# Optimization experiments

Hardware: AMD Instinct MI355X
Metric: run time of the kernel (lower is better)

Reference implementation:

```python
import jax, jax.numpy as jnp
import numpy as np

WEIGHT = 1.0
EPS = 1e-10


def _high_mask(h, w):
    # Boolean mask: True = high-frequency region (outside center rectangle after fftshift)
    mask = np.ones((h, w), dtype=np.float32)
    ch, cw = h // 2, w // 2
    mask[ch - h // 8: ch + h // 8, cw - w // 8: cw + w // 8] = 0.0
    return jnp.asarray(mask)


def _high_freq_psd(img):
    # img: (B, 3, H, W) in [-1, 1] -> per-image mean log10 PSD over high-freq region, shape (B,)
    gray = 0.299 * img[:, 0] + 0.587 * img[:, 1] + 0.114 * img[:, 2]  # (B, H, W)
    gray = (gray + 1.0) / 2.0
    fft = jnp.fft.fft2(gray)                       # batched complex FFT over last two dims
    fft = jnp.fft.fftshift(fft, axes=(-2, -1))
    psd_log = jnp.log10(jnp.abs(fft) ** 2 + EPS)   # (B, H, W)
    h, w = gray.shape[-2:]
    mask = _high_mask(h, w)
    return jnp.sum(psd_log * mask, axis=(-2, -1)) / jnp.sum(mask)


def setup_inputs() -> dict:
    key = jax.random.key(0)
    k1, k2 = jax.random.split(key)
    B, C, H, W = 32, 3, 512, 512
    generated = jax.random.normal(k1, (B, C, H, W), dtype=jnp.float32)
    target = jax.random.normal(k2, (B, C, H, W), dtype=jnp.float32)
    return {"generated": generated, "target": target}


def reference(generated, target):
    psd_gen = _high_freq_psd(generated)      # (B,)
    psd_target = _high_freq_psd(target)      # (B,)
    loss = jnp.mean(jnp.abs(psd_gen - psd_target))  # F.l1_loss
    return WEIGHT * loss
```

## Files before the change

kernel.cpp:

```cpp
#include <hip/hip_runtime.h>
#include <hip/hip_bf16.h>
#include <math.h>


__device__ double g_partials[64 * 33 * 4];
__device__ __align__(16) float2 g_wsfall[256 * 512];

__device__ __forceinline__ float2 cadd(float2 a, float2 b){ return make_float2(a.x+b.x, a.y+b.y); }
__device__ __forceinline__ float2 csub(float2 a, float2 b){ return make_float2(a.x-b.x, a.y-b.y); }
__device__ __forceinline__ float2 cmul(float2 a, float2 b){
  return make_float2(fmaf(a.x, b.x, -(a.y*b.y)), fmaf(a.x, b.y, a.y*b.x));
}
__device__ __forceinline__ float2 mul_mi(float2 a){ return make_float2(a.y, -a.x); }

__device__ __forceinline__ void fft8(float2 v[8]){
  const float S = 0.70710678118654752440f;
  float2 c0=cadd(v[0],v[4]), c1=cadd(v[1],v[5]), c2=cadd(v[2],v[6]), c3=cadd(v[3],v[7]);
  float2 d0=csub(v[0],v[4]);
  float2 t1=csub(v[1],v[5]);
  float2 d1=make_float2(S*(t1.x+t1.y), S*(t1.y-t1.x));
  float2 d2=mul_mi(csub(v[2],v[6]));
  float2 t3=csub(v[3],v[7]);
  float2 d3=make_float2(S*(t3.y-t3.x), -S*(t3.x+t3.y));
  float2 e0=cadd(c0,c2), e1=cadd(c1,c3), f0=csub(c0,c2), f1=mul_mi(csub(c1,c3));
  float2 g0=cadd(d0,d2), g1=cadd(d1,d3), h0=csub(d0,d2), h1=mul_mi(csub(d1,d3));
  v[0]=cadd(e0,e1); v[4]=csub(e0,e1);
  v[2]=cadd(f0,f1); v[6]=csub(f0,f1);
  v[1]=cadd(g0,g1); v[5]=csub(g0,g1);
  v[3]=cadd(h0,h1); v[7]=csub(h0,h1);
}

__device__ __forceinline__ void twiddle8(float2 v[8], float ang){
  float sn, cs;
  __sincosf(ang, &sn, &cs);
  float2 w = make_float2(cs, sn);
  float2 wp = w;
  v[1] = cmul(v[1], wp);
  #pragma unroll
  for (int m = 2; m < 8; ++m){ wp = cmul(wp, w); v[m] = cmul(v[m], wp); }
}

__device__ __forceinline__ int padi(int i){ return i + (i >> 3); }

__device__ __forceinline__ void lds_fence(){
  asm volatile("s_waitcnt lgkmcnt(0)" ::: "memory");
  __builtin_amdgcn_sched_barrier(0);
}

__device__ __forceinline__ void fft512(float2 v[8], float* re, float* im, int t){
  const float TW = -6.28318530717958647692f;
  fft8(v);
  twiddle8(v, TW * (float)t * (1.0f/512.0f));
  lds_fence();
  #pragma unroll
  for (int m = 0; m < 8; ++m){ int a = padi(m*64 + t); re[a] = v[m].x; im[a] = v[m].y; }
  lds_fence();
  const int q = t >> 3, n = t & 7;
  #pragma unroll
  for (int j = 0; j < 8; ++j){ int a = padi(q*64 + n + 8*j); v[j].x = re[a]; v[j].y = im[a]; }
  fft8(v);
  twiddle8(v, TW * (float)n * (1.0f/64.0f));
  lds_fence();
  #pragma unroll
  for (int m = 0; m < 8; ++m){ int a = padi(q*64 + m*8 + n); re[a] = v[m].x; im[a] = v[m].y; }
  lds_fence();
  #pragma unroll
  for (int j = 0; j < 8; ++j){ int a = padi(q*64 + n*8 + j); v[j].x = re[a]; v[j].y = im[a]; }
  fft8(v);
}

#define GRAY1(r,g,b) ((fmaf(0.299f,(r), fmaf(0.587f,(g), 0.114f*(b))) + 1.0f)*0.5f)

__global__ __launch_bounds__(256, 4)
void k_rowfft(const float* __restrict__ gen, const float* __restrict__ tgt,
              float2* ws, int img0){
  float2* w = ws ? ws : g_wsfall;
  const int wg   = blockIdx.x;
  const int imgl = wg >> 6;
  const int rg   = wg & 63;
  const int img  = img0 + imgl;
  const int wave = threadIdx.x >> 6, t = threadIdx.x & 63;
  const int pr   = rg*4 + wave;
  const float* src = (img < 32) ? gen : tgt;
  const float4* f4 = (const float4*)(src + (size_t)(img & 31) * 786432) + (size_t)pr * 256 + t;

  __shared__ float re_all[4][576], im_all[4][576];
  float* re = re_all[wave];
  float* im = im_all[wave];

  float4 aR0 = f4[0],          aR1 = f4[64];
  float4 bR0 = f4[128],        bR1 = f4[192];
  float4 aG0 = f4[65536],      aG1 = f4[65536+64];
  float4 bG0 = f4[65536+128],  bG1 = f4[65536+192];
  float4 aB0 = f4[131072],     aB1 = f4[131072+64];
  float4 bB0 = f4[131072+128], bB1 = f4[131072+192];

  const int x0 = 4*t, x1 = 256 + 4*t;
  re[padi(x0+0)] = GRAY1(aR0.x, aG0.x, aB0.x);
  re[padi(x0+1)] = GRAY1(aR0.y, aG0.y, aB0.y);
  re[padi(x0+2)] = GRAY1(aR0.z, aG0.z, aB0.z);
  re[padi(x0+3)] = GRAY1(aR0.w, aG0.w, aB0.w);
  re[padi(x1+0)] = GRAY1(aR1.x, aG1.x, aB1.x);
  re[padi(x1+1)] = GRAY1(aR1.y, aG1.y, aB1.y);
  re[padi(x1+2)] = GRAY1(aR1.z, aG1.z, aB1.z);
  re[padi(x1+3)] = GRAY1(aR1.w, aG1.w, aB1.w);
  im[padi(x0+0)] = GRAY1(bR0.x, bG0.x, bB0.x);
  im[padi(x0+1)] = GRAY1(bR0.y, bG0.y, bB0.y);
  im[padi(x0+2)] = GRAY1(bR0.z, bG0.z, bB0.z);
  im[padi(x0+3)] = GRAY1(bR0.w, bG0.w, bB0.w);
  im[padi(x1+0)] = GRAY1(bR1.x, bG1.x, bB1.x);
  im[padi(x1+1)] = GRAY1(bR1.y, bG1.y, bB1.y);
  im[padi(x1+2)] = GRAY1(bR1.z, bG1.z, bB1.z);
  im[padi(x1+3)] = GRAY1(bR1.w, bG1.w, bB1.w);
  lds_fence();

  float2 v[8];
  #pragma unroll
  for (int j = 0; j < 8; ++j){
    const int a = padi(t + 64*j);
    v[j].x = re[a];
    v[j].y = im[a];
  }
  fft512(v, re, im, t);

  float2* dst = w + ((size_t)imgl * 256 + pr) * 512;
  const int off = 8*(t & 7) + (t >> 3);
  #pragma unroll
  for (int j = 0; j < 8; ++j) dst[64*j + off] = v[j];
}

__global__ __launch_bounds__(256)
void k_colfft(const float2* __restrict__ ws, int img0){
  const float2* w = ws ? ws : (const float2*)g_wsfall;
  const int wg   = blockIdx.x;
  const int imgl = wg / 33;
  const int blk  = wg - imgl * 33;
  const int img  = img0 + imgl;
  const int kx0  = blk * 8;
  const int tid  = threadIdx.x;
  const int wave = tid >> 6, t = tid & 63;
  const int ncols = (blk == 32) ? 1 : 8;

  __shared__ float2 own[8][260], mir[8][260];
  __shared__ float re_all[4][576], im_all[4][576];
  float* re = re_all[wave];
  float* im = im_all[wave];

  const float2* zb = w + (size_t)imgl * 131072;
  #pragma unroll
  for (int it = 0; it < 8; ++it){
    const int idx = it*256 + tid;
    const int p = idx >> 3, e = idx & 7;
    own[e][p] = zb[p*512 + kx0 + e];
    mir[e][p] = zb[p*512 + ((512 - (kx0 + e)) & 511)];
  }
  __syncthreads();

  double acc = 0.0;
  for (int ci = 0; ci < 2; ++ci){
    const int e = wave*2 + ci;
    if (e < ncols){
      const int kx = kx0 + e;
      const bool sub_own = (kx <= 63);
      const bool sub_mir = (kx >= 1) & (kx <= 64);
      const float base = (kx == 0 || kx == 256) ? 1.0f : 2.0f;

      float2 v[8];
      const int u = t >> 1;
      const bool odd = (t & 1);
      #pragma unroll
      for (int j = 0; j < 8; ++j){
        const int p = u + 32*j;
        float2 A = own[e][p];
        float2 B = mir[e][p]; B.y = -B.y;
        float2 Fe = make_float2((A.x + B.x)*0.5f, (A.y + B.y)*0.5f);
        float2 Fo = mul_mi(make_float2((A.x - B.x)*0.5f, (A.y - B.y)*0.5f));
        v[j] = odd ? Fo : Fe;
      }
      fft512(v, re, im, t);

      #pragma unroll
      for (int j = 0; j < 8; ++j){
        const bool inS  = (j == 0) | (j == 7);
        const bool inSp = (j == 0) | ((j == 1) & (t == 0)) | ((j == 7) & (t != 0));
        float wgt = base;
        if (sub_own & inS)  wgt -= 1.0f;
        if (sub_mir & inSp) wgt -= 1.0f;
        float m2 = fmaf(v[j].x, v[j].x, fmaf(v[j].y, v[j].y, 1e-10f));
        acc += (double)wgt * (double)log10f(m2);
      }
    }
  }
  #pragma unroll
  for (int off = 32; off; off >>= 1) acc += __shfl_down(acc, off);
  if (t == 0) g_partials[((size_t)img * 33 + blk) * 4 + wave] = acc;
}

__global__ __launch_bounds__(256)
void k_finish(float* __restrict__ out){
  const int tid = threadIdx.x;
  const int img = tid >> 2, part = tid & 3;
  const double* p = g_partials + (size_t)img * 132 + part;
  double s = 0.0;
  for (int k = 0; k < 33; ++k) s += p[4*k];
  __shared__ double sm[256];
  sm[tid] = s;
  __syncthreads();
  if ((tid & 3) == 0){
    double tot = sm[tid] + sm[tid+1] + sm[tid+2] + sm[tid+3];
    sm[tid] = tot * (1.0 / 245760.0);
  }
  __syncthreads();
  if (tid < 64){
    double dv = (tid < 32) ? fabs(sm[tid*4] - sm[(tid+32)*4]) : 0.0;
    #pragma unroll
    for (int off = 32; off; off >>= 1) dv += __shfl_down(dv, off);
    if (tid == 0) out[0] = (float)(dv * (1.0 / 32.0));
  }
}

extern "C" void kernel_launch(void* const* d_in, const int* in_sizes, int n_in,
                              void* d_out, int out_size, void* d_ws, size_t ws_size,
                              hipStream_t stream){
  (void)in_sizes; (void)n_in; (void)out_size;
  const float* gen = (const float*)d_in[0];
  const float* tgt = (const float*)d_in[1];
  float* out = (float*)d_out;

  const size_t per_img = (size_t)256 * 512 * sizeof(float2);
  int chunk = (int)(ws_size / per_img);
  float2* wsp = (float2*)d_ws;
  if (chunk < 1){ chunk = 1; wsp = nullptr; }
  if (chunk > 64) chunk = 64;

  for (int i0 = 0; i0 < 64; i0 += chunk){
    const int n = (64 - i0 < chunk) ? (64 - i0) : chunk;
    k_rowfft<<<dim3(n * 64), dim3(256), 0, stream>>>(gen, tgt, wsp, i0);
    k_colfft<<<dim3(n * 33), dim3(256), 0, stream>>>(wsp, i0);
  }
  k_finish<<<dim3(1), dim3(256), 0, stream>>>(out);
}
```

Before: 76.23 us.

## Process two row pairs per wave in row FFT with shared twiddles

The row-FFT kernel now has each wave transform two packed complex row pairs at once through a dual fft512, sharing one sincos per stage across both. Grayscale results are written to LDS with vectorized float4 stores. The grid is halved and launch bounds drop to 2 blocks per SM. The aim is more instruction-level parallelism and more outstanding global loads per wave, with less twiddle computation and fewer blocks to launch. The cost is higher register and LDS use per block, which lowers occupancy. The column kernel only inlines its FFT using the new twiddle helper.

```diff
diff --git a/kernel.cpp b/kernel.cpp
--- a/kernel.cpp
+++ b/kernel.cpp
@@ -30,10 +30,7 @@
   v[3]=cadd(h0,h1); v[7]=csub(h0,h1);
 }
 
-__device__ __forceinline__ void twiddle8(float2 v[8], float ang){
-  float sn, cs;
-  __sincosf(ang, &sn, &cs);
-  float2 w = make_float2(cs, sn);
+__device__ __forceinline__ void twiddle8w(float2 v[8], float2 w){
   float2 wp = w;
   v[1] = cmul(v[1], wp);
   #pragma unroll
@@ -47,86 +44,114 @@
   __builtin_amdgcn_sched_barrier(0);
 }
 
-__device__ __forceinline__ void fft512(float2 v[8], float* re, float* im, int t){
+__device__ __forceinline__ void fft512x2(float2 va[8], float2 vb[8],
+                                         float* rea, float* ima,
+                                         float* reb, float* imb, int t){
   const float TW = -6.28318530717958647692f;
-  fft8(v);
-  twiddle8(v, TW * (float)t * (1.0f/512.0f));
-  lds_fence();
-  #pragma unroll
-  for (int m = 0; m < 8; ++m){ int a = padi(m*64 + t); re[a] = v[m].x; im[a] = v[m].y; }
+  float sn, cs;
+  fft8(va); fft8(vb);
+  __sincosf(TW * (float)t * (1.0f/512.0f), &sn, &cs);
+  { float2 w = make_float2(cs, sn); twiddle8w(va, w); twiddle8w(vb, w); }
+  lds_fence();
+  #pragma unroll
+  for (int m = 0; m < 8; ++m){
+    int a = padi(m*64 + t);
+    rea[a] = va[m].x; ima[a] = va[m].y;
+    reb[a] = vb[m].x; imb[a] = vb[m].y;
+  }
   lds_fence();
   const int q = t >> 3, n = t & 7;
   #pragma unroll
-  for (int j = 0; j < 8; ++j){ int a = padi(q*64 + n + 8*j); v[j].x = re[a]; v[j].y = im[a]; }
-  fft8(v);
-  twiddle8(v, TW * (float)n * (1.0f/64.0f));
-  lds_fence();
-  #pragma unroll
-  for (int m = 0; m < 8; ++m){ int a = padi(q*64 + m*8 + n); re[a] = v[m].x; im[a] = v[m].y; }
-  lds_fence();
-  #pragma unroll
-  for (int j = 0; j < 8; ++j){ int a = padi(q*64 + n*8 + j); v[j].x = re[a]; v[j].y = im[a]; }
-  fft8(v);
+  for (int j = 0; j < 8; ++j){
+    int a = padi(q*64 + n + 8*j);
+    va[j].x = rea[a]; va[j].y = ima[a];
+    vb[j].x = reb[a]; vb[j].y = imb[a];
+  }
+  fft8(va); fft8(vb);
+  __sincosf(TW * (float)n * (1.0f/64.0f), &sn, &cs);
+  { float2 w = make_float2(cs, sn); twiddle8w(va, w); twiddle8w(vb, w); }
+  lds_fence();
+  #pragma unroll
+  for (int m = 0; m < 8; ++m){
+    int a = padi(q*64 + m*8 + n);
+    rea[a] = va[m].x; ima[a] = va[m].y;
+    reb[a] = vb[m].x; imb[a] = vb[m].y;
+  }
+  lds_fence();
+  #pragma unroll
+  for (int j = 0; j < 8; ++j){
+    int a = padi(q*64 + n*8 + j);
+    va[j].x = rea[a]; va[j].y = ima[a];
+    vb[j].x = reb[a]; vb[j].y = imb[a];
+  }
+  fft8(va); fft8(vb);
 }
 
 #define GRAY1(r,g,b) ((fmaf(0.299f,(r), fmaf(0.587f,(g), 0.114f*(b))) + 1.0f)*0.5f)
-
-__global__ __launch_bounds__(256, 4)
+__device__ __forceinline__ float4 gray4(float4 r, float4 g, float4 b){
+  return make_float4(GRAY1(r.x,g.x,b.x), GRAY1(r.y,g.y,b.y),
+                     GRAY1(r.z,g.z,b.z), GRAY1(r.w,g.w,b.w));
+}
+
+__global__ __launch_bounds__(256, 2)
 void k_rowfft(const float* __restrict__ gen, const float* __restrict__ tgt,
               float2* ws, int img0){
   float2* w = ws ? ws : g_wsfall;
   const int wg   = blockIdx.x;
-  const int imgl = wg >> 6;
-  const int rg   = wg & 63;
+  const int imgl = wg >> 5;
+  const int rg   = wg & 31;
   const int img  = img0 + imgl;
   const int wave = threadIdx.x >> 6, t = threadIdx.x & 63;
-  const int pr   = rg*4 + wave;
+  const int prA  = rg*8 + wave*2;
+  const int prB  = prA + 1;
   const float* src = (img < 32) ? gen : tgt;
-  const float4* f4 = (const float4*)(src + (size_t)(img & 31) * 786432) + (size_t)pr * 256 + t;
-
-  __shared__ float re_all[4][576], im_all[4][576];
-  float* re = re_all[wave];
-  float* im = im_all[wave];
-
-  float4 aR0 = f4[0],          aR1 = f4[64];
-  float4 bR0 = f4[128],        bR1 = f4[192];
-  float4 aG0 = f4[65536],      aG1 = f4[65536+64];
-  float4 bG0 = f4[65536+128],  bG1 = f4[65536+192];
-  float4 aB0 = f4[131072],     aB1 = f4[131072+64];
-  float4 bB0 = f4[131072+128], bB1 = f4[131072+192];
-
-  const int x0 = 4*t, x1 = 256 + 4*t;
-  re[padi(x0+0)] = GRAY1(aR0.x, aG0.x, aB0.x);
-  re[padi(x0+1)] = GRAY1(aR0.y, aG0.y, aB0.y);
-  re[padi(x0+2)] = GRAY1(aR0.z, aG0.z, aB0.z);
-  re[padi(x0+3)] = GRAY1(aR0.w, aG0.w, aB0.w);
-  re[padi(x1+0)] = GRAY1(aR1.x, aG1.x, aB1.x);
-  re[padi(x1+1)] = GRAY1(aR1.y, aG1.y, aB1.y);
-  re[padi(x1+2)] = GRAY1(aR1.z, aG1.z, aB1.z);
-  re[padi(x1+3)] = GRAY1(aR1.w, aG1.w, aB1.w);
-  im[padi(x0+0)] = GRAY1(bR0.x, bG0.x, bB0.x);
-  im[padi(x0+1)] = GRAY1(bR0.y, bG0.y, bB0.y);
-  im[padi(x0+2)] = GRAY1(bR0.z, bG0.z, bB0.z);
-  im[padi(x0+3)] = GRAY1(bR0.w, bG0.w, bB0.w);
-  im[padi(x1+0)] = GRAY1(bR1.x, bG1.x, bB1.x);
-  im[padi(x1+1)] = GRAY1(bR1.y, bG1.y, bB1.y);
-  im[padi(x1+2)] = GRAY1(bR1.z, bG1.z, bB1.z);
-  im[padi(x1+3)] = GRAY1(bR1.w, bG1.w, bB1.w);
-  lds_fence();
-
-  float2 v[8];
-  #pragma unroll
-  for (int j = 0; j < 8; ++j){
-    const int a = padi(t + 64*j);
-    v[j].x = re[a];
-    v[j].y = im[a];
-  }
-  fft512(v, re, im, t);
-
-  float2* dst = w + ((size_t)imgl * 256 + pr) * 512;
+  const float4* f4 = (const float4*)(src + (size_t)(img & 31) * 786432);
+  const float4* fA = f4 + (size_t)prA * 256 + t;
+  const float4* fB = f4 + (size_t)prB * 256 + t;
+
+  __shared__ float ex[4][4][576];
+  float* reA = ex[wave][0]; float* imA = ex[wave][1];
+  float* reB = ex[wave][2]; float* imB = ex[wave][3];
+
+  float4 ArR0 = fA[0],             ArR1 = fA[64];
+  float4 AsR0 = fA[128],           AsR1 = fA[192];
+  float4 ArG0 = fA[65536],         ArG1 = fA[65536+64];
+  float4 AsG0 = fA[65536+128],     AsG1 = fA[65536+192];
+  float4 ArB0 = fA[131072],        ArB1 = fA[131072+64];
+  float4 AsB0 = fA[131072+128],    AsB1 = fA[131072+192];
+  float4 BrR0 = fB[0],             BrR1 = fB[64];
+  float4 BsR0 = fB[128],           BsR1 = fB[192];
+  float4 BrG0 = fB[65536],         BrG1 = fB[65536+64];
+  float4 BsG0 = fB[65536+128],     BsG1 = fB[65536+192];
+  float4 BrB0 = fB[131072],        BrB1 = fB[131072+64];
+  float4 BsB0 = fB[131072+128],    BsB1 = fB[131072+192];
+
+  ((float4*)reA)[t]      = gray4(ArR0, ArG0, ArB0);
+  ((float4*)reA)[64 + t] = gray4(ArR1, ArG1, ArB1);
+  ((float4*)imA)[t]      = gray4(AsR0, AsG0, AsB0);
+  ((float4*)imA)[64 + t] = gray4(AsR1, AsG1, AsB1);
+  ((float4*)reB)[t]      = gray4(BrR0, BrG0, BrB0);
+  ((float4*)reB)[64 + t] = gray4(BrR1, BrG1, BrB1);
+  ((float4*)imB)[t]      = gray4(BsR0, BsG0, BsB0);
+  ((float4*)imB)[64 + t] = gray4(BsR1, BsG1, BsB1);
+  lds_fence();
+
+  float2 va[8], vb[8];
+  #pragma unroll
+  for (int j = 0; j < 8; ++j){
+    va[j] = make_float2(reA[t + 64*j], imA[t + 64*j]);
+    vb[j] = make_float2(reB[t + 64*j], imB[t + 64*j]);
+  }
+  fft512x2(va, vb, reA, imA, reB, imB, t);
+
+  float2* dstA = w + ((size_t)imgl * 256 + prA) * 512;
+  float2* dstB = w + ((size_t)imgl * 256 + prB) * 512;
   const int off = 8*(t & 7) + (t >> 3);
   #pragma unroll
-  for (int j = 0; j < 8; ++j) dst[64*j + off] = v[j];
+  for (int j = 0; j < 8; ++j){
+    dstA[64*j + off] = va[j];
+    dstB[64*j + off] = vb[j];
+  }
 }
 
 __global__ __launch_bounds__(256)
@@ -156,6 +181,7 @@
   }
   __syncthreads();
 
+  const float TW = -6.28318530717958647692f;
   double acc = 0.0;
   for (int ci = 0; ci < 2; ++ci){
     const int e = wave*2 + ci;
@@ -177,7 +203,29 @@
         float2 Fo = mul_mi(make_float2((A.x - B.x)*0.5f, (A.y - B.y)*0.5f));
         v[j] = odd ? Fo : Fe;
       }
-      fft512(v, re, im, t);
+      {
+        float sn, cs;
+        fft8(v);
+        __sincosf(TW * (float)t * (1.0f/512.0f), &sn, &cs);
+        { float2 wtw = make_float2(cs, sn); twiddle8w(v, wtw); }
+        lds_fence();
+        #pragma unroll
+        for (int m = 0; m < 8; ++m){ int a = padi(m*64 + t); re[a] = v[m].x; im[a] = v[m].y; }
+        lds_fence();
+        const int q = t >> 3, n = t & 7;
+        #pragma unroll
+        for (int j = 0; j < 8; ++j){ int a = padi(q*64 + n + 8*j); v[j].x = re[a]; v[j].y = im[a]; }
+        fft8(v);
+        __sincosf(TW * (float)n * (1.0f/64.0f), &sn, &cs);
+        { float2 wtw = make_float2(cs, sn); twiddle8w(v, wtw); }
+        lds_fence();
+        #pragma unroll
+        for (int m = 0; m < 8; ++m){ int a = padi(q*64 + m*8 + n); re[a] = v[m].x; im[a] = v[m].y; }
+        lds_fence();
+        #pragma unroll
+        for (int j = 0; j < 8; ++j){ int a = padi(q*64 + n*8 + j); v[j].x = re[a]; v[j].y = im[a]; }
+        fft8(v);
+      }
 
       #pragma unroll
       for (int j = 0; j < 8; ++j){
@@ -235,7 +283,7 @@
 
   for (int i0 = 0; i0 < 64; i0 += chunk){
     const int n = (64 - i0 < chunk) ? (64 - i0) : chunk;
-    k_rowfft<<<dim3(n * 64), dim3(256), 0, stream>>>(gen, tgt, wsp, i0);
+    k_rowfft<<<dim3(n * 32), dim3(256), 0, stream>>>(gen, tgt, wsp, i0);
     k_colfft<<<dim3(n * 33), dim3(256), 0, stream>>>(wsp, i0);
   }
   k_finish<<<dim3(1), dim3(256), 0, stream>>>(out);
```

After: 76.14 us. No clear change (-0.1%).
